# Performance work log

Measured on AMD Instinct MI355X. Metric: run time of the kernel, lower is better.

Reference implementation:

```python
import jax, jax.numpy as jnp
import numpy as np

N_NODES = 10000
N_EDGES = 160000
NUM_FEAT = 14
DIM = 256


def gat_conv(x, src, dst, W, a_s, a_d, b, concat):
    """PyG GATConv: W [H*C, F_in], a_s/a_d [H, C], edges src->dst (self-loops included)."""
    H, C = a_s.shape
    N = x.shape[0]
    h = (x @ W.T).reshape(N, H, C)                       # [N,H,C]
    alpha_src = (h * a_s).sum(-1)                        # [N,H]
    alpha_dst = (h * a_d).sum(-1)                        # [N,H]
    e = jax.nn.leaky_relu(alpha_src[src] + alpha_dst[dst], negative_slope=0.2)  # [E,H]
    emax = jax.ops.segment_max(e, dst, num_segments=N)   # [N,H]
    emax = jnp.where(jnp.isneginf(emax), 0.0, emax)
    ex = jnp.exp(e - emax[dst])
    denom = jax.ops.segment_sum(ex, dst, num_segments=N)
    coef = ex / (denom[dst] + 1e-16)                     # segment softmax over in-edges
    out = jax.ops.segment_sum(h[src] * coef[..., None], dst, num_segments=N)  # [N,H,C]
    out = out.reshape(N, H * C) if concat else out.mean(axis=1)
    return out + b


def setup_inputs() -> dict:
    key = jax.random.key(0)
    ks = jax.random.split(key, 24)
    d = DIM
    f = NUM_FEAT
    def w(k, shape, fan_in):
        return jax.random.normal(k, shape, dtype=jnp.float32) * (1.0 / np.sqrt(fan_in))
    inp = {
        "x": jax.random.normal(ks[0], (N_NODES, f), dtype=jnp.float32),
        "edge_index": jax.random.randint(ks[1], (2, N_EDGES), 0, N_NODES, dtype=jnp.int64
                                         if jax.config.jax_enable_x64 else jnp.int32),
        # conv1: 14 -> 4 heads x 256
        "W1": w(ks[2], (4 * d, f), f),
        "a1s": w(ks[3], (4, d), d), "a1d": w(ks[4], (4, d), d),
        "b1": jnp.zeros((4 * d,), jnp.float32),
        "lw1": w(ks[5], (4 * d, f), f), "lb1": jnp.zeros((4 * d,), jnp.float32),
        # conv2: 1024 -> 4 heads x 256
        "W2": w(ks[6], (4 * d, 4 * d), 4 * d),
        "a2s": w(ks[7], (4, d), d), "a2d": w(ks[8], (4, d), d),
        "b2": jnp.zeros((4 * d,), jnp.float32),
        "lw2": w(ks[9], (4 * d, 4 * d), 4 * d), "lb2": jnp.zeros((4 * d,), jnp.float32),
        # conv3: 1024 -> 6 heads x 256, mean over heads
        "W3": w(ks[10], (6 * d, 4 * d), 4 * d),
        "a3s": w(ks[11], (6, d), d), "a3d": w(ks[12], (6, d), d),
        "b3": jnp.zeros((d,), jnp.float32),
        "lw3": w(ks[13], (d, 4 * d), 4 * d), "lb3": jnp.zeros((d,), jnp.float32),
    }
    return inp


def reference(x, edge_index, W1, a1s, a1d, b1, lw1, lb1,
              W2, a2s, a2d, b2, lw2, lb2,
              W3, a3s, a3d, b3, lw3, lb3):
    N = x.shape[0]
    loops = jnp.arange(N, dtype=edge_index.dtype)
    src = jnp.concatenate([edge_index[0], loops])
    dst = jnp.concatenate([edge_index[1], loops])
    x1 = jax.nn.elu(gat_conv(x, src, dst, W1, a1s, a1d, b1, True) + x @ lw1.T + lb1)
    x2 = jax.nn.elu(gat_conv(x1, src, dst, W2, a2s, a2d, b2, True) + x1 @ lw2.T + lb2)
    x3 = gat_conv(x2, src, dst, W3, a3s, a3d, b3, False) + x2 @ lw3.T + lb3
    return x3
```

## Files before the change

kernel.cpp:

```cpp
#include <hip/hip_runtime.h>
#include <hip/hip_bf16.h>
#include <cstddef>

#define NN 10000
#define EE0 160000
#define NF 14
#define DC 256

static inline int ceildiv(int a, int b) { return (a + b - 1) / b; }

__device__ __forceinline__ float lrelu02(float x) { return fmaxf(x, 0.2f * x); }

__device__ __forceinline__ short f2bf(float f) {
    unsigned u = __float_as_uint(f);
    unsigned r = (u + 0x7FFFu + ((u >> 16) & 1u)) >> 16;
    return (short)r;
}
__device__ __forceinline__ float bf2f(short s) {
    return __uint_as_float(((unsigned)(unsigned short)s) << 16);
}

typedef __attribute__((ext_vector_type(8))) short bf16x8;
typedef __attribute__((ext_vector_type(4))) float f32x4;

#define GLDS(gaddr, laddr)                                                         \
    __builtin_amdgcn_global_load_lds(                                              \
        (__attribute__((address_space(1))) void*)(gaddr),                          \
        (__attribute__((address_space(3))) void*)(laddr), 16, 0, 0)

__global__ void count_edges_k(const int* __restrict__ ei, int* __restrict__ counts,
                              int E0, int N) {
    int e = blockIdx.x * 256 + threadIdx.x;
    int E = E0 + N;
    if (e >= E) return;
    int dst = (e < E0) ? ei[E0 + e] : (e - E0);
    atomicAdd(&counts[dst], 1);
}

__global__ __launch_bounds__(1024) void scan_k(const int* __restrict__ counts,
                                               int* __restrict__ row_off, int n) {
    __shared__ int sums[1024];
    int t = threadIdx.x;
    int chunk = (n + 1023) >> 10;
    int base = t * chunk;
    int lim = base + chunk; if (lim > n) lim = n;
    int s = 0;
    for (int i = base; i < lim; ++i) s += counts[i];
    sums[t] = s;
    __syncthreads();
    for (int off = 1; off < 1024; off <<= 1) {
        int v = (t >= off) ? sums[t - off] : 0;
        __syncthreads();
        sums[t] += v;
        __syncthreads();
    }
    int run = (t == 0) ? 0 : sums[t - 1];
    for (int i = base; i < lim; ++i) { run += counts[i]; row_off[i + 1] = run; }
    if (t == 0) row_off[0] = 0;
}

__global__ void scatter_k(const int* __restrict__ ei, const int* __restrict__ row_off,
                          int* __restrict__ cursor, int* __restrict__ csr_src,
                          int E0, int N) {
    int e = blockIdx.x * 256 + threadIdx.x;
    int E = E0 + N;
    if (e >= E) return;
    int src, dst;
    if (e < E0) { src = ei[e]; dst = ei[E0 + e]; }
    else        { src = dst = e - E0; }
    int pos = row_off[dst] + atomicAdd(&cursor[dst], 1);
    csr_src[pos] = src;
}

__global__ __launch_bounds__(256) void cvt_bf16_fused_k(
    const float* __restrict__ p0, short* __restrict__ q0, int n0,
    const float* __restrict__ p1, short* __restrict__ q1, int n1,
    const float* __restrict__ p2, short* __restrict__ q2, int n2,
    const float* __restrict__ p3, short* __restrict__ q3, int n3) {
    int i = blockIdx.x * 256 + threadIdx.x;
    const float* in; short* out; int idx;
    if (i < n0) { in = p0; out = q0; idx = i; }
    else if (i < n0 + n1) { in = p1; out = q1; idx = i - n0; }
    else if (i < n0 + n1 + n2) { in = p2; out = q2; idx = i - n0 - n1; }
    else if (i < n0 + n1 + n2 + n3) { in = p3; out = q3; idx = i - n0 - n1 - n2; }
    else return;
    float4 v = ((const float4*)in)[idx];
    short4 o;
    o.x = f2bf(v.x); o.y = f2bf(v.y); o.z = f2bf(v.z); o.w = f2bf(v.w);
    ((short4*)out)[idx] = o;
}

__global__ __launch_bounds__(256) void pad_bf16_k(
    const float* __restrict__ p0, short* __restrict__ q0, int r0,
    const float* __restrict__ p1, short* __restrict__ q1, int r1,
    const float* __restrict__ p2, short* __restrict__ q2, int r2,
    int K, int Kp) {
    int i = blockIdx.x * 256 + threadIdx.x;
    int rows = r0 + r1 + r2;
    int total = rows * Kp;
    if (i >= total) return;
    int row = i / Kp, col = i - row * Kp;
    const float* in; short* out; int r;
    if (row < r0) { in = p0; out = q0; r = row; }
    else if (row < r0 + r1) { in = p1; out = q1; r = row - r0; }
    else { in = p2; out = q2; r = row - r0 - r1; }
    out[(size_t)r * Kp + col] = (col < K) ? f2bf(in[(size_t)r * K + col]) : (short)0;
}

__global__ __launch_bounds__(256) void gemm_bf16_dual(
    const short* __restrict__ A, const short* __restrict__ B,
    const float* __restrict__ b1, const float* __restrict__ b2,
    const float* __restrict__ a_s, const float* __restrict__ a_d,
    float* __restrict__ ps, float* __restrict__ pd,
    short* __restrict__ Cb, void* __restrict__ Cf, int lin_bf16,
    int M, int Nh, int Nf, int K, int H) {
    __shared__ short As[2][128 * 32];
    __shared__ short Bs[2][128 * 32];
    const int t = threadIdx.x;
    const int wave = t >> 6, lane = t & 63;
    const int m0 = blockIdx.y * 128, n0 = blockIdx.x * 128;
    const int wm = (wave >> 1) * 64, wn = (wave & 1) * 64;
    const int lane15 = lane & 15, quad = lane >> 4;

    const int lrow = lane >> 2;
    const int lk = ((lane & 3) ^ ((lrow >> 1) & 3)) * 8;
    int arow0 = m0 + wave * 16 + lrow;
    int arow1 = arow0 + 64;
    if (arow0 > M - 1) arow0 = M - 1;
    if (arow1 > M - 1) arow1 = M - 1;
    const short* ag0 = A + (size_t)arow0 * K + lk;
    const short* ag1 = A + (size_t)arow1 * K + lk;
    const short* bg0 = B + (size_t)(n0 + wave * 16 + lrow) * K + lk;
    const short* bg1 = B + (size_t)(n0 + 64 + wave * 16 + lrow) * K + lk;
    const int alo0 = (wave * 16) * 32;
    const int alo1 = (64 + wave * 16) * 32;

    const int rql = (quad ^ ((lane15 >> 1) & 3)) * 8;

    f32x4 acc[4][4];
#pragma unroll
    for (int i = 0; i < 4; ++i)
#pragma unroll
        for (int j = 0; j < 4; ++j) acc[i][j] = (f32x4){0.f, 0.f, 0.f, 0.f};

    for (int k0 = 0; k0 < K; k0 += 64) {
        GLDS(ag0 + k0, &As[0][alo0]);
        GLDS(ag1 + k0, &As[0][alo1]);
        GLDS(bg0 + k0, &Bs[0][alo0]);
        GLDS(bg1 + k0, &Bs[0][alo1]);
        const bool two = (k0 + 32 < K);
        if (two) {
            GLDS(ag0 + k0 + 32, &As[1][alo0]);
            GLDS(ag1 + k0 + 32, &As[1][alo1]);
            GLDS(bg0 + k0 + 32, &Bs[1][alo0]);
            GLDS(bg1 + k0 + 32, &Bs[1][alo1]);
        }
        __syncthreads();
        {
            bf16x8 af[4], bfr[4];
#pragma unroll
            for (int i = 0; i < 4; ++i)
                af[i] = *(const bf16x8*)&As[0][(wm + 16 * i + lane15) * 32 + rql];
#pragma unroll
            for (int j = 0; j < 4; ++j)
                bfr[j] = *(const bf16x8*)&Bs[0][(wn + 16 * j + lane15) * 32 + rql];
#pragma unroll
            for (int i = 0; i < 4; ++i)
#pragma unroll
                for (int j = 0; j < 4; ++j)
                    acc[i][j] = __builtin_amdgcn_mfma_f32_16x16x32_bf16(
                        af[i], bfr[j], acc[i][j], 0, 0, 0);
        }
        if (two) {
            bf16x8 af[4], bfr[4];
#pragma unroll
            for (int i = 0; i < 4; ++i)
                af[i] = *(const bf16x8*)&As[1][(wm + 16 * i + lane15) * 32 + rql];
#pragma unroll
            for (int j = 0; j < 4; ++j)
                bfr[j] = *(const bf16x8*)&Bs[1][(wn + 16 * j + lane15) * 32 + rql];
#pragma unroll
            for (int i = 0; i < 4; ++i)
#pragma unroll
                for (int j = 0; j < 4; ++j)
                    acc[i][j] = __builtin_amdgcn_mfma_f32_16x16x32_bf16(
                        af[i], bfr[j], acc[i][j], 0, 0, 0);
        }
        __syncthreads();
    }

    if (n0 >= Nh) {
#pragma unroll
        for (int j = 0; j < 4; ++j) {
            int nc = n0 - Nh + wn + 16 * j + lane15;
            float bias = b1[nc] + b2[nc];
#pragma unroll
            for (int i = 0; i < 4; ++i) {
                int mb = m0 + wm + 16 * i + quad * 4;
#pragma unroll
                for (int r = 0; r < 4; ++r) {
                    int m = mb + r;
                    if (m < M) {
                        float v = acc[i][j][r] + bias;
                        if (lin_bf16) ((short*)Cf)[(size_t)m * Nf + nc] = f2bf(v);
                        else          ((float*)Cf)[(size_t)m * Nf + nc] = v;
                    }
                }
            }
        }
    } else {
        const int chunk = (n0 + wn) >> 6;
        const int head = chunk >> 2;
        const int cb = (n0 + wn) & 255;
        float asv[4], adv[4];
#pragma unroll
        for (int j = 0; j < 4; ++j) {
            asv[j] = a_s[head * DC + cb + 16 * j + lane15];
            adv[j] = a_d[head * DC + cb + 16 * j + lane15];
        }
#pragma unroll
        for (int j = 0; j < 4; ++j) {
            int n = n0 + wn + 16 * j + lane15;
#pragma unroll
            for (int i = 0; i < 4; ++i) {
                int mb = m0 + wm + 16 * i + quad * 4;
#pragma unroll
                for (int r = 0; r < 4; ++r) {
                    int m = mb + r;
                    if (m < M) Cb[(size_t)m * Nh + n] = f2bf(acc[i][j][r]);
                }
            }
        }
        float* psc = ps + (size_t)chunk * M;
        float* pdc = pd + (size_t)chunk * M;
#pragma unroll
        for (int i = 0; i < 4; ++i) {
#pragma unroll
            for (int r = 0; r < 4; ++r) {
                float s = acc[i][0][r] * asv[0] + acc[i][1][r] * asv[1] +
                          acc[i][2][r] * asv[2] + acc[i][3][r] * asv[3];
                float d = acc[i][0][r] * adv[0] + acc[i][1][r] * adv[1] +
                          acc[i][2][r] * adv[2] + acc[i][3][r] * adv[3];
#pragma unroll
                for (int off = 8; off > 0; off >>= 1) {
                    s += __shfl_xor(s, off);
                    d += __shfl_xor(d, off);
                }
                int m = m0 + wm + 16 * i + quad * 4 + r;
                if (lane15 == 0 && m < M) { psc[m] = s; pdc[m] = d; }
            }
        }
    }
}

__global__ __launch_bounds__(256) void alpha_reduce_k(
    const float* __restrict__ ps, const float* __restrict__ pd,
    float* __restrict__ asrc, float* __restrict__ adst, int M, int H) {
    int m = blockIdx.x * 256 + threadIdx.x;
    int h = blockIdx.y;
    if (m >= M) return;
    float s = 0.f, d = 0.f;
#pragma unroll
    for (int c = 0; c < 4; ++c) {
        s += ps[(size_t)(h * 4 + c) * M + m];
        d += pd[(size_t)(h * 4 + c) * M + m];
    }
    asrc[m * H + h] = s;
    adst[m * H + h] = d;
}

__global__ __launch_bounds__(256) void gat_agg(
    const short* __restrict__ hbuf, const short* __restrict__ lin,
    const float* __restrict__ asrc, const float* __restrict__ adst_a,
    const int* __restrict__ row_off, const int* __restrict__ csr_src,
    short* __restrict__ outx, int N, int H) {
    int wid = (int)((blockIdx.x * (size_t)blockDim.x + threadIdx.x) >> 6);
    int lane = threadIdx.x & 63;
    int HP = H >> 1;
    if (wid >= N * HP) return;
    int n = wid / HP, hp = wid - n * HP;
    int hA = hp * 2;
    int beg = row_off[n], end = row_off[n + 1];
    int deg = end - beg;
    const float2 adp = *(const float2*)(adst_a + (size_t)n * H + hA);
    const bool loH = (lane < 32);

    size_t cbase = (size_t)n * (H * DC) + (size_t)hA * DC + lane * 8;
    float acc[8];
    {
        bf16x8 lv = *(const bf16x8*)(lin + cbase);
#pragma unroll
        for (int j = 0; j < 8; ++j) acc[j] = bf2f(lv[j]);
    }
    const size_t hoff = (size_t)hA * DC + lane * 8;

    if (deg <= 64) {
        int s = 0; float eA = -1e38f, eB = -1e38f;
        if (lane < deg) {
            s = csr_src[beg + lane];
            float2 av = *(const float2*)(asrc + (size_t)s * H + hA);
            eA = lrelu02(av.x + adp.x);
            eB = lrelu02(av.y + adp.y);
        }
        float mA = eA, mB = eB;
#pragma unroll
        for (int off = 32; off > 0; off >>= 1) {
            mA = fmaxf(mA, __shfl_xor(mA, off));
            mB = fmaxf(mB, __shfl_xor(mB, off));
        }
        float pA = (lane < deg) ? __expf(eA - mA) : 0.f;
        float pB = (lane < deg) ? __expf(eB - mB) : 0.f;
        float sA = pA, sB = pB;
#pragma unroll
        for (int off = 32; off > 0; off >>= 1) {
            sA += __shfl_xor(sA, off);
            sB += __shfl_xor(sB, off);
        }
        float coefA = pA / (sA + 1e-16f);
        float coefB = pB / (sB + 1e-16f);

        int i = 0;
        for (; i + 8 <= deg; i += 8) {
            bf16x8 v[8]; float w[8];
#pragma unroll
            for (int u = 0; u < 8; ++u) {
                int su = __shfl(s, i + u);
                v[u] = *(const bf16x8*)(hbuf + (size_t)su * (H * DC) + hoff);
                float wA = __shfl(coefA, i + u);
                float wB = __shfl(coefB, i + u);
                w[u] = loH ? wA : wB;
            }
#pragma unroll
            for (int u = 0; u < 8; ++u)
#pragma unroll
                for (int j = 0; j < 8; ++j) acc[j] += w[u] * bf2f(v[u][j]);
        }
        for (; i < deg; ++i) {
            int si = __shfl(s, i);
            float wA = __shfl(coefA, i);
            float wB = __shfl(coefB, i);
            float wv = loH ? wA : wB;
            const bf16x8 hv = *(const bf16x8*)(hbuf + (size_t)si * (H * DC) + hoff);
#pragma unroll
            for (int j = 0; j < 8; ++j) acc[j] += wv * bf2f(hv[j]);
        }
    } else {
        float mA = -1e38f, mB = -1e38f;
        for (int i = beg + lane; i < end; i += 64) {
            int s = csr_src[i];
            float2 av = *(const float2*)(asrc + (size_t)s * H + hA);
            mA = fmaxf(mA, lrelu02(av.x + adp.x));
            mB = fmaxf(mB, lrelu02(av.y + adp.y));
        }
#pragma unroll
        for (int off = 32; off > 0; off >>= 1) {
            mA = fmaxf(mA, __shfl_xor(mA, off));
            mB = fmaxf(mB, __shfl_xor(mB, off));
        }
        float sA = 0.f, sB = 0.f;
        for (int i = beg + lane; i < end; i += 64) {
            int s = csr_src[i];
            float2 av = *(const float2*)(asrc + (size_t)s * H + hA);
            sA += __expf(lrelu02(av.x + adp.x) - mA);
            sB += __expf(lrelu02(av.y + adp.y) - mB);
        }
#pragma unroll
        for (int off = 32; off > 0; off >>= 1) {
            sA += __shfl_xor(sA, off);
            sB += __shfl_xor(sB, off);
        }
        float invA = 1.f / (sA + 1e-16f);
        float invB = 1.f / (sB + 1e-16f);
        for (int i = beg; i < end; ++i) {
            int s = csr_src[i];
            float2 av = *(const float2*)(asrc + (size_t)s * H + hA);
            float wA = __expf(lrelu02(av.x + adp.x) - mA) * invA;
            float wB = __expf(lrelu02(av.y + adp.y) - mB) * invB;
            float wv = loH ? wA : wB;
            const bf16x8 hv = *(const bf16x8*)(hbuf + (size_t)s * (H * DC) + hoff);
#pragma unroll
            for (int j = 0; j < 8; ++j) acc[j] += wv * bf2f(hv[j]);
        }
    }
    bf16x8 o;
#pragma unroll
    for (int j = 0; j < 8; ++j) {
        float a = acc[j];
        a = a > 0.f ? a : __expf(a) - 1.f;
        o[j] = f2bf(a);
    }
    *(bf16x8*)(outx + cbase) = o;
}

__global__ __launch_bounds__(192) void gat_agg_mean(
    const short* __restrict__ hbuf, const float* __restrict__ asrc,
    const float* __restrict__ adst_a, const int* __restrict__ row_off,
    const int* __restrict__ csr_src, float* __restrict__ out, int N) {
    const int H = 6;
    __shared__ float red[6][DC];
    int n = blockIdx.x;
    int wave = threadIdx.x >> 6, lane = threadIdx.x & 63;
    int hA = wave * 2;
    int beg = row_off[n], end = row_off[n + 1];
    int deg = end - beg;
    const float invH = 1.f / 6.f;
    const float2 adp = *(const float2*)(adst_a + (size_t)n * H + hA);
    const bool loH = (lane < 32);

    float acc[8];
#pragma unroll
    for (int j = 0; j < 8; ++j) acc[j] = 0.f;
    const size_t hoff = (size_t)hA * DC + lane * 8;

    if (deg <= 64) {
        int s = 0; float eA = -1e38f, eB = -1e38f;
        if (lane < deg) {
            s = csr_src[beg + lane];
            float2 av = *(const float2*)(asrc + (size_t)s * H + hA);
            eA = lrelu02(av.x + adp.x);
            eB = lrelu02(av.y + adp.y);
        }
        float mA = eA, mB = eB;
#pragma unroll
        for (int off = 32; off > 0; off >>= 1) {
            mA = fmaxf(mA, __shfl_xor(mA, off));
            mB = fmaxf(mB, __shfl_xor(mB, off));
        }
        float pA = (lane < deg) ? __expf(eA - mA) : 0.f;
        float pB = (lane < deg) ? __expf(eB - mB) : 0.f;
        float sA = pA, sB = pB;
#pragma unroll
        for (int off = 32; off > 0; off >>= 1) {
            sA += __shfl_xor(sA, off);
            sB += __shfl_xor(sB, off);
        }
        float coefA = pA * invH / (sA + 1e-16f);
        float coefB = pB * invH / (sB + 1e-16f);

        int i = 0;
        for (; i + 8 <= deg; i += 8) {
            bf16x8 v[8]; float w[8];
#pragma unroll
            for (int u = 0; u < 8; ++u) {
                int su = __shfl(s, i + u);
                v[u] = *(const bf16x8*)(hbuf + (size_t)su * (H * DC) + hoff);
                float wA = __shfl(coefA, i + u);
                float wB = __shfl(coefB, i + u);
                w[u] = loH ? wA : wB;
            }
#pragma unroll
            for (int u = 0; u < 8; ++u)
#pragma unroll
                for (int j = 0; j < 8; ++j) acc[j] += w[u] * bf2f(v[u][j]);
        }
        for (; i < deg; ++i) {
            int si = __shfl(s, i);
            float wA = __shfl(coefA, i);
            float wB = __shfl(coefB, i);
            float wv = loH ? wA : wB;
            const bf16x8 hv = *(const bf16x8*)(hbuf + (size_t)si * (H * DC) + hoff);
#pragma unroll
            for (int j = 0; j < 8; ++j) acc[j] += wv * bf2f(hv[j]);
        }
    } else {
        float mA = -1e38f, mB = -1e38f;
        for (int i = beg + lane; i < end; i += 64) {
            int s = csr_src[i];
            float2 av = *(const float2*)(asrc + (size_t)s * H + hA);
            mA = fmaxf(mA, lrelu02(av.x + adp.x));
            mB = fmaxf(mB, lrelu02(av.y + adp.y));
        }
#pragma unroll
        for (int off = 32; off > 0; off >>= 1) {
            mA = fmaxf(mA, __shfl_xor(mA, off));
            mB = fmaxf(mB, __shfl_xor(mB, off));
        }
        float sA = 0.f, sB = 0.f;
        for (int i = beg + lane; i < end; i += 64) {
            int s = csr_src[i];
            float2 av = *(const float2*)(asrc + (size_t)s * H + hA);
            sA += __expf(lrelu02(av.x + adp.x) - mA);
            sB += __expf(lrelu02(av.y + adp.y) - mB);
        }
#pragma unroll
        for (int off = 32; off > 0; off >>= 1) {
            sA += __shfl_xor(sA, off);
            sB += __shfl_xor(sB, off);
        }
        float invA = invH / (sA + 1e-16f);
        float invB = invH / (sB + 1e-16f);
        for (int i = beg; i < end; ++i) {
            int s = csr_src[i];
            float2 av = *(const float2*)(asrc + (size_t)s * H + hA);
            float wA = __expf(lrelu02(av.x + adp.x) - mA) * invA;
            float wB = __expf(lrelu02(av.y + adp.y) - mB) * invB;
            float wv = loH ? wA : wB;
            const bf16x8 hv = *(const bf16x8*)(hbuf + (size_t)s * (H * DC) + hoff);
#pragma unroll
            for (int j = 0; j < 8; ++j) acc[j] += wv * bf2f(hv[j]);
        }
    }
    {
        int head = hA + (loH ? 0 : 1);
        int ch0 = (lane & 31) * 8;
        *(float4*)&red[head][ch0]     = make_float4(acc[0], acc[1], acc[2], acc[3]);
        *(float4*)&red[head][ch0 + 4] = make_float4(acc[4], acc[5], acc[6], acc[7]);
    }
    __syncthreads();
    if (wave == 0) {
        float* op = out + (size_t)n * DC + lane * 4;
        float4 o = *(float4*)op;
#pragma unroll
        for (int j = 0; j < 6; ++j) {
            float4 r = *(float4*)&red[j][lane * 4];
            o.x += r.x; o.y += r.y; o.z += r.z; o.w += r.w;
        }
        *(float4*)op = o;
    }
}

extern "C" void kernel_launch(void* const* d_in, const int* in_sizes, int n_in,
                              void* d_out, int out_size, void* d_ws, size_t ws_size,
                              hipStream_t stream) {
    const float* x   = (const float*)d_in[0];
    const int*   ei  = (const int*)d_in[1];
    const float* W1  = (const float*)d_in[2];
    const float* a1s = (const float*)d_in[3];
    const float* a1d = (const float*)d_in[4];
    const float* b1  = (const float*)d_in[5];
    const float* lw1 = (const float*)d_in[6];
    const float* lb1 = (const float*)d_in[7];
    const float* W2  = (const float*)d_in[8];
    const float* a2s = (const float*)d_in[9];
    const float* a2d = (const float*)d_in[10];
    const float* b2  = (const float*)d_in[11];
    const float* lb2_w = (const float*)d_in[12];
    const float* lb2 = (const float*)d_in[13];
    const float* W3  = (const float*)d_in[14];
    const float* a3s = (const float*)d_in[15];
    const float* a3d = (const float*)d_in[16];
    const float* b3  = (const float*)d_in[17];
    const float* lw3 = (const float*)d_in[18];
    const float* lb3 = (const float*)d_in[19];
    const float* lw2 = lb2_w;
    float* out = (float*)d_out;

    const int N = NN, E0 = EE0, E = EE0 + NN;

    unsigned char* w = (unsigned char*)d_ws;
    size_t off = 0;
    auto alloc = [&](size_t bytes) {
        void* p = w + off;
        off += (bytes + 255) & ~(size_t)255;
        return p;
    };
    short* hbuf   = (short*)alloc((size_t)N * 1536 * 2);
    short* buf    = (short*)alloc((size_t)N * 1024 * 2);
    short* xb     = (short*)alloc((size_t)N * 1024 * 2);
    short* xpad   = (short*)alloc((size_t)N * 32 * 2);
    short* W1p    = (short*)alloc((size_t)1024 * 32 * 2);
    short* lw1p   = (short*)alloc((size_t)1024 * 32 * 2);
    short* W2b    = (short*)alloc((size_t)1024 * 1024 * 2);
    short* lw2b   = (short*)alloc((size_t)1024 * 1024 * 2);
    short* W3b    = (short*)alloc((size_t)1536 * 1024 * 2);
    short* lw3b   = (short*)alloc((size_t)256 * 1024 * 2);
    float* psrc   = (float*)alloc((size_t)24 * N * 4);
    float* pdst   = (float*)alloc((size_t)24 * N * 4);
    float* asrc   = (float*)alloc((size_t)N * 6 * 4);
    float* adst   = (float*)alloc((size_t)N * 6 * 4);
    int* row_off  = (int*)alloc((size_t)(N + 1) * 4);
    int* counts2  = (int*)alloc((size_t)2 * N * 4);
    int* counts   = counts2;
    int* cursor   = counts2 + N;
    int* csr_src  = (int*)alloc((size_t)E * 4);
    (void)ws_size; (void)n_in; (void)in_sizes; (void)out_size;

    hipMemsetAsync(counts2, 0, (size_t)2 * N * 4, stream);
    count_edges_k<<<ceildiv(E, 256), 256, 0, stream>>>(ei, counts, E0, N);
    scan_k<<<1, 1024, 0, stream>>>(counts, row_off, N);
    scatter_k<<<ceildiv(E, 256), 256, 0, stream>>>(ei, row_off, cursor, csr_src, E0, N);

    {
        int q0 = 1024 * 1024 / 4, q1 = 1024 * 1024 / 4, q2 = 1536 * 1024 / 4,
            q3 = 256 * 1024 / 4;
        cvt_bf16_fused_k<<<ceildiv(q0 + q1 + q2 + q3, 256), 256, 0, stream>>>(
            W2, W2b, q0, lw2, lw2b, q1, W3, W3b, q2, lw3, lw3b, q3);
        int rows = N + 1024 + 1024;
        pad_bf16_k<<<ceildiv(rows * 32, 256), 256, 0, stream>>>(
            x, xpad, N, W1, W1p, 1024, lw1, lw1p, 1024, NF, 32);
    }

    gemm_bf16_dual<<<dim3(16, ceildiv(N, 128)), 256, 0, stream>>>(
        xpad, W1p, b1, lb1, a1s, a1d, psrc, pdst, hbuf, (void*)buf, 1,
        N, 1024, 1024, 32, 4);
    alpha_reduce_k<<<dim3(ceildiv(N, 256), 4), 256, 0, stream>>>(
        psrc, pdst, asrc, adst, N, 4);
    gat_agg<<<ceildiv(N * 2, 4), 256, 0, stream>>>(hbuf, buf, asrc, adst, row_off,
                                                   csr_src, xb, N, 4);

    gemm_bf16_dual<<<dim3(16, ceildiv(N, 128)), 256, 0, stream>>>(
        xb, W2b, b2, lb2, a2s, a2d, psrc, pdst, hbuf, (void*)buf, 1,
        N, 1024, 1024, 1024, 4);
    alpha_reduce_k<<<dim3(ceildiv(N, 256), 4), 256, 0, stream>>>(
        psrc, pdst, asrc, adst, N, 4);
    gat_agg<<<ceildiv(N * 2, 4), 256, 0, stream>>>(hbuf, buf, asrc, adst, row_off,
                                                   csr_src, xb, N, 4);

    gemm_bf16_dual<<<dim3(14, ceildiv(N, 128)), 256, 0, stream>>>(
        xb, W3b, b3, lb3, a3s, a3d, psrc, pdst, hbuf, (void*)out, 0,
        N, 1536, 256, 1024, 6);
    alpha_reduce_k<<<dim3(ceildiv(N, 256), 6), 256, 0, stream>>>(
        psrc, pdst, asrc, adst, N, 6);
    gat_agg_mean<<<N, 192, 0, stream>>>(hbuf, asrc, adst, row_off, csr_src, out, N);
}
```

Before: 487.3 us.

## Split softmax coefficients into separate kernel and simplify GEMM k-loop staging

Attention coefficients are now computed by a dedicated coef_k kernel and stored per edge and head-pair in a new float2 buffer. The aggregation kernels then stream those precomputed weights alongside source indices, so they no longer do the softmax, the shuffles, or the serial high-degree path. This costs an extra launch and a write plus read of the coefficient buffer per layer. Separately, the GEMM main loop now stages one 32-wide K slice per barrier instead of two, which halves shared memory but doubles the number of synchronisations.

```diff
diff --git a/kernel.cpp b/kernel.cpp
--- a/kernel.cpp
+++ b/kernel.cpp
@@ -114,8 +114,8 @@
     float* __restrict__ ps, float* __restrict__ pd,
     short* __restrict__ Cb, void* __restrict__ Cf, int lin_bf16,
     int M, int Nh, int Nf, int K, int H) {
-    __shared__ short As[2][128 * 32];
-    __shared__ short Bs[2][128 * 32];
+    __shared__ short As[128 * 32];
+    __shared__ short Bs[128 * 32];
     const int t = threadIdx.x;
     const int wave = t >> 6, lane = t & 63;
     const int m0 = blockIdx.y * 128, n0 = blockIdx.x * 128;
@@ -132,8 +132,10 @@
     const short* ag1 = A + (size_t)arow1 * K + lk;
     const short* bg0 = B + (size_t)(n0 + wave * 16 + lrow) * K + lk;
     const short* bg1 = B + (size_t)(n0 + 64 + wave * 16 + lrow) * K + lk;
-    const int alo0 = (wave * 16) * 32;
-    const int alo1 = (64 + wave * 16) * 32;
+    short* al0 = &As[(wave * 16) * 32];
+    short* al1 = &As[(64 + wave * 16) * 32];
+    short* bl0 = &Bs[(wave * 16) * 32];
+    short* bl1 = &Bs[(64 + wave * 16) * 32];
 
     const int rql = (quad ^ ((lane15 >> 1) & 3)) * 8;
 
@@ -143,49 +145,25 @@
 #pragma unroll
         for (int j = 0; j < 4; ++j) acc[i][j] = (f32x4){0.f, 0.f, 0.f, 0.f};
 
-    for (int k0 = 0; k0 < K; k0 += 64) {
-        GLDS(ag0 + k0, &As[0][alo0]);
-        GLDS(ag1 + k0, &As[0][alo1]);
-        GLDS(bg0 + k0, &Bs[0][alo0]);
-        GLDS(bg1 + k0, &Bs[0][alo1]);
-        const bool two = (k0 + 32 < K);
-        if (two) {
-            GLDS(ag0 + k0 + 32, &As[1][alo0]);
-            GLDS(ag1 + k0 + 32, &As[1][alo1]);
-            GLDS(bg0 + k0 + 32, &Bs[1][alo0]);
-            GLDS(bg1 + k0 + 32, &Bs[1][alo1]);
-        }
+    for (int k0 = 0; k0 < K; k0 += 32) {
+        GLDS(ag0 + k0, al0);
+        GLDS(ag1 + k0, al1);
+        GLDS(bg0 + k0, bl0);
+        GLDS(bg1 + k0, bl1);
         __syncthreads();
-        {
-            bf16x8 af[4], bfr[4];
-#pragma unroll
-            for (int i = 0; i < 4; ++i)
-                af[i] = *(const bf16x8*)&As[0][(wm + 16 * i + lane15) * 32 + rql];
+        bf16x8 af[4], bfr[4];
+#pragma unroll
+        for (int i = 0; i < 4; ++i)
+            af[i] = *(const bf16x8*)&As[(wm + 16 * i + lane15) * 32 + rql];
+#pragma unroll
+        for (int j = 0; j < 4; ++j)
+            bfr[j] = *(const bf16x8*)&Bs[(wn + 16 * j + lane15) * 32 + rql];
+#pragma unroll
+        for (int i = 0; i < 4; ++i)
 #pragma unroll
             for (int j = 0; j < 4; ++j)
-                bfr[j] = *(const bf16x8*)&Bs[0][(wn + 16 * j + lane15) * 32 + rql];
-#pragma unroll
-            for (int i = 0; i < 4; ++i)
-#pragma unroll
-                for (int j = 0; j < 4; ++j)
-                    acc[i][j] = __builtin_amdgcn_mfma_f32_16x16x32_bf16(
-                        af[i], bfr[j], acc[i][j], 0, 0, 0);
-        }
-        if (two) {
-            bf16x8 af[4], bfr[4];
-#pragma unroll
-            for (int i = 0; i < 4; ++i)
-                af[i] = *(const bf16x8*)&As[1][(wm + 16 * i + lane15) * 32 + rql];
-#pragma unroll
-            for (int j = 0; j < 4; ++j)
-                bfr[j] = *(const bf16x8*)&Bs[1][(wn + 16 * j + lane15) * 32 + rql];
-#pragma unroll
-            for (int i = 0; i < 4; ++i)
-#pragma unroll
-                for (int j = 0; j < 4; ++j)
-                    acc[i][j] = __builtin_amdgcn_mfma_f32_16x16x32_bf16(
-                        af[i], bfr[j], acc[i][j], 0, 0, 0);
-        }
+                acc[i][j] = __builtin_amdgcn_mfma_f32_16x16x32_bf16(
+                    af[i], bfr[j], acc[i][j], 0, 0, 0);
         __syncthreads();
     }
 
@@ -269,11 +247,10 @@
     adst[m * H + h] = d;
 }
 
-__global__ __launch_bounds__(256) void gat_agg(
-    const short* __restrict__ hbuf, const short* __restrict__ lin,
+__global__ __launch_bounds__(256) void coef_k(
     const float* __restrict__ asrc, const float* __restrict__ adst_a,
     const int* __restrict__ row_off, const int* __restrict__ csr_src,
-    short* __restrict__ outx, int N, int H) {
+    float2* __restrict__ cp, int N, int H, int E) {
     int wid = (int)((blockIdx.x * (size_t)blockDim.x + threadIdx.x) >> 6);
     int lane = threadIdx.x & 63;
     int HP = H >> 1;
@@ -283,16 +260,7 @@
     int beg = row_off[n], end = row_off[n + 1];
     int deg = end - beg;
     const float2 adp = *(const float2*)(adst_a + (size_t)n * H + hA);
-    const bool loH = (lane < 32);
-
-    size_t cbase = (size_t)n * (H * DC) + (size_t)hA * DC + lane * 8;
-    float acc[8];
-    {
-        bf16x8 lv = *(const bf16x8*)(lin + cbase);
-#pragma unroll
-        for (int j = 0; j < 8; ++j) acc[j] = bf2f(lv[j]);
-    }
-    const size_t hoff = (size_t)hA * DC + lane * 8;
+    float2* cpp = cp + (size_t)hp * E;
 
     if (deg <= 64) {
         int s = 0; float eA = -1e38f, eB = -1e38f;
@@ -316,34 +284,8 @@
             sA += __shfl_xor(sA, off);
             sB += __shfl_xor(sB, off);
         }
-        float coefA = pA / (sA + 1e-16f);
-        float coefB = pB / (sB + 1e-16f);
-
-        int i = 0;
-        for (; i + 8 <= deg; i += 8) {
-            bf16x8 v[8]; float w[8];
-#pragma unroll
-            for (int u = 0; u < 8; ++u) {
-                int su = __shfl(s, i + u);
-                v[u] = *(const bf16x8*)(hbuf + (size_t)su * (H * DC) + hoff);
-                float wA = __shfl(coefA, i + u);
-                float wB = __shfl(coefB, i + u);
-                w[u] = loH ? wA : wB;
-            }
-#pragma unroll
-            for (int u = 0; u < 8; ++u)
-#pragma unroll
-                for (int j = 0; j < 8; ++j) acc[j] += w[u] * bf2f(v[u][j]);
-        }
-        for (; i < deg; ++i) {
-            int si = __shfl(s, i);
-            float wA = __shfl(coefA, i);
-            float wB = __shfl(coefB, i);
-            float wv = loH ? wA : wB;
-            const bf16x8 hv = *(const bf16x8*)(hbuf + (size_t)si * (H * DC) + hoff);
-#pragma unroll
-            for (int j = 0; j < 8; ++j) acc[j] += wv * bf2f(hv[j]);
-        }
+        if (lane < deg)
+            cpp[beg + lane] = make_float2(pA / (sA + 1e-16f), pB / (sB + 1e-16f));
     } else {
         float mA = -1e38f, mB = -1e38f;
         for (int i = beg + lane; i < end; i += 64) {
@@ -371,16 +313,63 @@
         }
         float invA = 1.f / (sA + 1e-16f);
         float invB = 1.f / (sB + 1e-16f);
-        for (int i = beg; i < end; ++i) {
+        for (int i = beg + lane; i < end; i += 64) {
             int s = csr_src[i];
             float2 av = *(const float2*)(asrc + (size_t)s * H + hA);
-            float wA = __expf(lrelu02(av.x + adp.x) - mA) * invA;
-            float wB = __expf(lrelu02(av.y + adp.y) - mB) * invB;
-            float wv = loH ? wA : wB;
-            const bf16x8 hv = *(const bf16x8*)(hbuf + (size_t)s * (H * DC) + hoff);
-#pragma unroll
-            for (int j = 0; j < 8; ++j) acc[j] += wv * bf2f(hv[j]);
-        }
+            cpp[i] = make_float2(__expf(lrelu02(av.x + adp.x) - mA) * invA,
+                                 __expf(lrelu02(av.y + adp.y) - mB) * invB);
+        }
+    }
+}
+
+__global__ __launch_bounds__(256) void gat_agg(
+    const short* __restrict__ hbuf, const short* __restrict__ lin,
+    const float2* __restrict__ cp, const int* __restrict__ row_off,
+    const int* __restrict__ csr_src, short* __restrict__ outx,
+    int N, int H, int E) {
+    int wid = (int)((blockIdx.x * (size_t)blockDim.x + threadIdx.x) >> 6);
+    int lane = threadIdx.x & 63;
+    int HP = H >> 1;
+    if (wid >= N * HP) return;
+    int n = wid / HP, hp = wid - n * HP;
+    int hA = hp * 2;
+    const int beg = __builtin_amdgcn_readfirstlane(row_off[n]);
+    const int end = __builtin_amdgcn_readfirstlane(row_off[n + 1]);
+    const bool loH = (lane < 32);
+
+    size_t cbase = (size_t)n * (H * DC) + (size_t)hA * DC + lane * 8;
+    float acc[8];
+    {
+        bf16x8 lv = *(const bf16x8*)(lin + cbase);
+#pragma unroll
+        for (int j = 0; j < 8; ++j) acc[j] = bf2f(lv[j]);
+    }
+    const size_t hoff = (size_t)hA * DC + lane * 8;
+    const float2* cpp = cp + (size_t)hp * E;
+
+    int i = beg;
+    for (; i + 8 <= end; i += 8) {
+        int su[8]; float2 w[8];
+#pragma unroll
+        for (int u = 0; u < 8; ++u) { su[u] = csr_src[i + u]; w[u] = cpp[i + u]; }
+        bf16x8 v[8];
+#pragma unroll
+        for (int u = 0; u < 8; ++u)
+            v[u] = *(const bf16x8*)(hbuf + (size_t)su[u] * (H * DC) + hoff);
+#pragma unroll
+        for (int u = 0; u < 8; ++u) {
+            float wv = loH ? w[u].x : w[u].y;
+#pragma unroll
+            for (int j = 0; j < 8; ++j) acc[j] += wv * bf2f(v[u][j]);
+        }
+    }
+    for (; i < end; ++i) {
+        int su = csr_src[i];
+        float2 wp = cpp[i];
+        float wv = loH ? wp.x : wp.y;
+        const bf16x8 hv = *(const bf16x8*)(hbuf + (size_t)su * (H * DC) + hoff);
+#pragma unroll
+        for (int j = 0; j < 8; ++j) acc[j] += wv * bf2f(hv[j]);
     }
     bf16x8 o;
 #pragma unroll
@@ -393,113 +382,51 @@
 }
 
 __global__ __launch_bounds__(192) void gat_agg_mean(
-    const short* __restrict__ hbuf, const float* __restrict__ asrc,
-    const float* __restrict__ adst_a, const int* __restrict__ row_off,
-    const int* __restrict__ csr_src, float* __restrict__ out, int N) {
+    const short* __restrict__ hbuf, const float2* __restrict__ cp,
+    const int* __restrict__ row_off, const int* __restrict__ csr_src,
+    float* __restrict__ out, int N, int E) {
     const int H = 6;
     __shared__ float red[6][DC];
     int n = blockIdx.x;
     int wave = threadIdx.x >> 6, lane = threadIdx.x & 63;
-    int hA = wave * 2;
-    int beg = row_off[n], end = row_off[n + 1];
-    int deg = end - beg;
+    int hp = wave, hA = hp * 2;
+    const int beg = __builtin_amdgcn_readfirstlane(row_off[n]);
+    const int end = __builtin_amdgcn_readfirstlane(row_off[n + 1]);
     const float invH = 1.f / 6.f;
-    const float2 adp = *(const float2*)(adst_a + (size_t)n * H + hA);
     const bool loH = (lane < 32);
 
     float acc[8];
 #pragma unroll
     for (int j = 0; j < 8; ++j) acc[j] = 0.f;
     const size_t hoff = (size_t)hA * DC + lane * 8;
-
-    if (deg <= 64) {
-        int s = 0; float eA = -1e38f, eB = -1e38f;
-        if (lane < deg) {
-            s = csr_src[beg + lane];
-            float2 av = *(const float2*)(asrc + (size_t)s * H + hA);
-            eA = lrelu02(av.x + adp.x);
-            eB = lrelu02(av.y + adp.y);
-        }
-        float mA = eA, mB = eB;
-#pragma unroll
-        for (int off = 32; off > 0; off >>= 1) {
-            mA = fmaxf(mA, __shfl_xor(mA, off));
-            mB = fmaxf(mB, __shfl_xor(mB, off));
-        }
-        float pA = (lane < deg) ? __expf(eA - mA) : 0.f;
-        float pB = (lane < deg) ? __expf(eB - mB) : 0.f;
-        float sA = pA, sB = pB;
-#pragma unroll
-        for (int off = 32; off > 0; off >>= 1) {
-            sA += __shfl_xor(sA, off);
-            sB += __shfl_xor(sB, off);
-        }
-        float coefA = pA * invH / (sA + 1e-16f);
-        float coefB = pB * invH / (sB + 1e-16f);
-
-        int i = 0;
-        for (; i + 8 <= deg; i += 8) {
-            bf16x8 v[8]; float w[8];
-#pragma unroll
-            for (int u = 0; u < 8; ++u) {
-                int su = __shfl(s, i + u);
-                v[u] = *(const bf16x8*)(hbuf + (size_t)su * (H * DC) + hoff);
-                float wA = __shfl(coefA, i + u);
-                float wB = __shfl(coefB, i + u);
-                w[u] = loH ? wA : wB;
-            }
-#pragma unroll
-            for (int u = 0; u < 8; ++u)
-#pragma unroll
-                for (int j = 0; j < 8; ++j) acc[j] += w[u] * bf2f(v[u][j]);
-        }
-        for (; i < deg; ++i) {
-            int si = __shfl(s, i);
-            float wA = __shfl(coefA, i);
-            float wB = __shfl(coefB, i);
-            float wv = loH ? wA : wB;
-            const bf16x8 hv = *(const bf16x8*)(hbuf + (size_t)si * (H * DC) + hoff);
-#pragma unroll
-            for (int j = 0; j < 8; ++j) acc[j] += wv * bf2f(hv[j]);
-        }
-    } else {
-        float mA = -1e38f, mB = -1e38f;
-        for (int i = beg + lane; i < end; i += 64) {
-            int s = csr_src[i];
-            float2 av = *(const float2*)(asrc + (size_t)s * H + hA);
-            mA = fmaxf(mA, lrelu02(av.x + adp.x));
-            mB = fmaxf(mB, lrelu02(av.y + adp.y));
-        }
-#pragma unroll
-        for (int off = 32; off > 0; off >>= 1) {
-            mA = fmaxf(mA, __shfl_xor(mA, off));
-            mB = fmaxf(mB, __shfl_xor(mB, off));
-        }
-        float sA = 0.f, sB = 0.f;
-        for (int i = beg + lane; i < end; i += 64) {
-            int s = csr_src[i];
-            float2 av = *(const float2*)(asrc + (size_t)s * H + hA);
-            sA += __expf(lrelu02(av.x + adp.x) - mA);
-            sB += __expf(lrelu02(av.y + adp.y) - mB);
-        }
-#pragma unroll
-        for (int off = 32; off > 0; off >>= 1) {
-            sA += __shfl_xor(sA, off);
-            sB += __shfl_xor(sB, off);
-        }
-        float invA = invH / (sA + 1e-16f);
-        float invB = invH / (sB + 1e-16f);
-        for (int i = beg; i < end; ++i) {
-            int s = csr_src[i];
-            float2 av = *(const float2*)(asrc + (size_t)s * H + hA);
-            float wA = __expf(lrelu02(av.x + adp.x) - mA) * invA;
-            float wB = __expf(lrelu02(av.y + adp.y) - mB) * invB;
-            float wv = loH ? wA : wB;
-            const bf16x8 hv = *(const bf16x8*)(hbuf + (size_t)s * (H * DC) + hoff);
-#pragma unroll
-            for (int j = 0; j < 8; ++j) acc[j] += wv * bf2f(hv[j]);
-        }
-    }
+    const float2* cpp = cp + (size_t)hp * E;
+
+    int i = beg;
+    for (; i + 8 <= end; i += 8) {
+        int su[8]; float2 w[8];
+#pragma unroll
+        for (int u = 0; u < 8; ++u) { su[u] = csr_src[i + u]; w[u] = cpp[i + u]; }
+        bf16x8 v[8];
+#pragma unroll
+        for (int u = 0; u < 8; ++u)
+            v[u] = *(const bf16x8*)(hbuf + (size_t)su[u] * (H * DC) + hoff);
+#pragma unroll
+        for (int u = 0; u < 8; ++u) {
+            float wv = loH ? w[u].x : w[u].y;
+#pragma unroll
+            for (int j = 0; j < 8; ++j) acc[j] += wv * bf2f(v[u][j]);
+        }
+    }
+    for (; i < end; ++i) {
+        int su = csr_src[i];
+        float2 wp = cpp[i];
+        float wv = loH ? wp.x : wp.y;
+        const bf16x8 hv = *(const bf16x8*)(hbuf + (size_t)su * (H * DC) + hoff);
+#pragma unroll
+        for (int j = 0; j < 8; ++j) acc[j] += wv * bf2f(hv[j]);
+    }
+#pragma unroll
+    for (int j = 0; j < 8; ++j) acc[j] *= invH;
     {
         int head = hA + (loH ? 0 : 1);
         int ch0 = (lane & 31) * 8;
@@ -568,6 +495,7 @@
     float* pdst   = (float*)alloc((size_t)24 * N * 4);
     float* asrc   = (float*)alloc((size_t)N * 6 * 4);
     float* adst   = (float*)alloc((size_t)N * 6 * 4);
+    float2* cp    = (float2*)alloc((size_t)3 * E * 8);
     int* row_off  = (int*)alloc((size_t)(N + 1) * 4);
     int* counts2  = (int*)alloc((size_t)2 * N * 4);
     int* counts   = counts2;
@@ -595,21 +523,27 @@
         N, 1024, 1024, 32, 4);
     alpha_reduce_k<<<dim3(ceildiv(N, 256), 4), 256, 0, stream>>>(
         psrc, pdst, asrc, adst, N, 4);
-    gat_agg<<<ceildiv(N * 2, 4), 256, 0, stream>>>(hbuf, buf, asrc, adst, row_off,
-                                                   csr_src, xb, N, 4);
+    coef_k<<<ceildiv(N * 2, 4), 256, 0, stream>>>(asrc, adst, row_off, csr_src,
+                                                  cp, N, 4, E);
+    gat_agg<<<ceildiv(N * 2, 4), 256, 0, stream>>>(hbuf, buf, cp, row_off,
+                                                   csr_src, xb, N, 4, E);
 
     gemm_bf16_dual<<<dim3(16, ceildiv(N, 128)), 256, 0, stream>>>(
         xb, W2b, b2, lb2, a2s, a2d, psrc, pdst, hbuf, (void*)buf, 1,
         N, 1024, 1024, 1024, 4);
     alpha_reduce_k<<<dim3(ceildiv(N, 256), 4), 256, 0, stream>>>(
         psrc, pdst, asrc, adst, N, 4);
-    gat_agg<<<ceildiv(N * 2, 4), 256, 0, stream>>>(hbuf, buf, asrc, adst, row_off,
-                                                   csr_src, xb, N, 4);
+    coef_k<<<ceildiv(N * 2, 4), 256, 0, stream>>>(asrc, adst, row_off, csr_src,
+                                                  cp, N, 4, E);
+    gat_agg<<<ceildiv(N * 2, 4), 256, 0, stream>>>(hbuf, buf, cp, row_off,
+                                                   csr_src, xb, N, 4, E);
 
     gemm_bf16_dual<<<dim3(14, ceildiv(N, 128)), 256, 0, stream>>>(
         xb, W3b, b3, lb3, a3s, a3d, psrc, pdst, hbuf, (void*)out, 0,
         N, 1536, 256, 1024, 6);
     alpha_reduce_k<<<dim3(ceildiv(N, 256), 6), 256, 0, stream>>>(
         psrc, pdst, asrc, adst, N, 6);
-    gat_agg_mean<<<N, 192, 0, stream>>>(hbuf, asrc, adst, row_off, csr_src, out, N);
-}
+    coef_k<<<ceildiv(N * 3, 4), 256, 0, stream>>>(asrc, adst, row_off, csr_src,
+                                                  cp, N, 6, E);
+    gat_agg_mean<<<N, 192, 0, stream>>>(hbuf, cp, row_off, csr_src, out, N, E);
+}
```

Measured after the change: 524.8 us. 7.7% more time.
